# Performance work log

Hardware: AMD Instinct MI355X
Metric: run time of the kernel (lower is better)

Reference implementation:

```python
import jax, jax.numpy as jnp
import numpy as np

S, B, H, F, E, K = 2048, 4, 1024, 4096, 8, 2


def setup_inputs() -> dict:
    key = jax.random.key(0)
    k1, k2, k3, k4 = jax.random.split(key, 4)
    scale_h = 1.0 / np.sqrt(H)
    scale_f = 1.0 / np.sqrt(F)
    return {
        "x": jax.random.normal(k1, (S, B, H), dtype=jnp.float32),
        "router_w": jax.random.normal(k2, (H, E), dtype=jnp.float32) * scale_h,
        "w1": jax.random.normal(k3, (E, H, F), dtype=jnp.float32) * scale_h,
        "w2": jax.random.normal(k4, (E, F, H), dtype=jnp.float32) * scale_f,
    }


def reference(x, router_w, w1, w2):
    # x: [S, B, H] (Megatron layout). Flatten to tokens.
    s, b, h = x.shape
    xt = x.reshape(-1, h)                       # [T, H], T = S*B
    # --- TopK router: softmax over expert logits, then top-k probs ---
    logits = xt @ router_w                      # [T, E]
    probs = jax.nn.softmax(logits, axis=-1)     # [T, E]
    top_p, top_i = jax.lax.top_k(probs, K)      # [T, K] each
    # --- Grouped-GEMM expert MLPs + weighted combine ---
    # Loop over the small fixed expert set; each expert applies fc1->gelu->fc2
    # to every token, masked/weighted by its routing probability (math is
    # identical to dispatch/permute/grouped-GEMM/combine in Megatron).
    out = jnp.zeros_like(xt)
    for e in range(E):
        gate_e = jnp.sum(jnp.where(top_i == e, top_p, 0.0), axis=-1)  # [T]
        hidden = jax.nn.gelu(xt @ w1[e], approximate=True)            # [T, F]
        out = out + gate_e[:, None] * (hidden @ w2[e])                # [T, H]
    return out.reshape(s, b, h)
```

## Files before the change

### kernel.cpp

```cpp
#include <hip/hip_runtime.h>
#include <cstdint>
#include <cstddef>

#define T_TOKENS 8192
#define H_DIM    1024
#define F_DIM    4096
#define E_NUM    8

typedef __bf16 bf16x8 __attribute__((ext_vector_type(8)));
typedef float  f32x4  __attribute__((ext_vector_type(4)));
typedef unsigned short ushort8 __attribute__((ext_vector_type(8)));

#define AS_GLOBAL(p) ((const __attribute__((address_space(1))) void*)(p))
#define AS_LDS(p)    ((__attribute__((address_space(3))) void*)(p))

__device__ inline unsigned short f2b(float f) {
  unsigned int u = __float_as_uint(f);
  unsigned int r = (u + 0x7fffu + ((u >> 16) & 1u)) >> 16;
  return (unsigned short)r;
}
__device__ inline float b2f(unsigned short u) {
  return __uint_as_float(((unsigned int)u) << 16);
}
__device__ inline float gelu_fast(float v) {
  float u2 = 1.5957691216057308f * v * (1.0f + 0.044715f * v * v);
  return v / (1.0f + __expf(-u2));
}

__global__ __launch_bounds__(256) void transpose_cast_kernel(
    const float* __restrict__ in, unsigned short* __restrict__ out, int R, int C)
{
  __shared__ float tile[64][65];
  const int e  = blockIdx.z;
  const int c0 = blockIdx.x * 64;
  const int r0 = blockIdx.y * 64;
  const float* src = in + (size_t)e * R * C;
  unsigned short* dst = out + (size_t)e * R * C;
  const int tid = threadIdx.x;
  const int rl  = tid >> 4;
  const int cl4 = (tid & 15) * 4;
#pragma unroll
  for (int i = 0; i < 4; ++i) {
    float4 v = *(const float4*)(src + (size_t)(r0 + rl + i * 16) * C + c0 + cl4);
    tile[rl + i * 16][cl4 + 0] = v.x;
    tile[rl + i * 16][cl4 + 1] = v.y;
    tile[rl + i * 16][cl4 + 2] = v.z;
    tile[rl + i * 16][cl4 + 3] = v.w;
  }
  __syncthreads();
  const int cl = tid >> 2;
  const int rb = (tid & 3) * 16;
#pragma unroll
  for (int j = 0; j < 4; ++j) {
    ushort4 u;
    u.x = f2b(tile[rb + j * 4 + 0][cl]);
    u.y = f2b(tile[rb + j * 4 + 1][cl]);
    u.z = f2b(tile[rb + j * 4 + 2][cl]);
    u.w = f2b(tile[rb + j * 4 + 3][cl]);
    *(ushort4*)(dst + (size_t)(c0 + cl) * R + r0 + rb + j * 4) = u;
  }
}

__global__ void zero_meta_kernel(int* __restrict__ counts) {
  if (threadIdx.x < 24) counts[threadIdx.x] = 0;
}

__global__ __launch_bounds__(256) void router_kernel(
    const float* __restrict__ x, const float* __restrict__ rw,
    unsigned short* __restrict__ xb, int* __restrict__ top_e, float* __restrict__ top_p,
    int* __restrict__ counts)
{
  __shared__ float lrw[H_DIM * 9];
  __shared__ int lc[E_NUM];
  const int tid = threadIdx.x;
  if (tid < E_NUM) lc[tid] = 0;
  for (int r = tid; r < H_DIM; r += 256) {
    const float* s = rw + r * 8;
    float4 a = *(const float4*)(s);
    float4 b = *(const float4*)(s + 4);
    float* d = &lrw[r * 9];
    d[0] = a.x; d[1] = a.y; d[2] = a.z; d[3] = a.w;
    d[4] = b.x; d[5] = b.y; d[6] = b.z; d[7] = b.w;
  }
  __syncthreads();
  const int lane = tid & 63, wid = tid >> 6;
  for (int i = 0; i < 8; ++i) {
    const int t = blockIdx.x * 32 + wid * 8 + i;
    float acc[8] = {0.f, 0.f, 0.f, 0.f, 0.f, 0.f, 0.f, 0.f};
    const float* xrow = x + (size_t)t * H_DIM;
    unsigned short* xbrow = xb + (size_t)t * H_DIM;
#pragma unroll
    for (int j = 0; j < 16; ++j) {
      int h = j * 64 + lane;
      float xv = xrow[h];
      xbrow[h] = f2b(xv);
      const float* rr = &lrw[h * 9];
#pragma unroll
      for (int e = 0; e < 8; ++e) acc[e] += xv * rr[e];
    }
#pragma unroll
    for (int e = 0; e < 8; ++e) {
#pragma unroll
      for (int s = 32; s > 0; s >>= 1) acc[e] += __shfl_xor(acc[e], s, 64);
    }
    if (lane == 0) {
      float mx = acc[0];
      for (int e = 1; e < 8; ++e) mx = fmaxf(mx, acc[e]);
      float p[8]; float sum = 0.f;
      for (int e = 0; e < 8; ++e) { p[e] = expf(acc[e] - mx); sum += p[e]; }
      float inv = 1.0f / sum;
      int i1 = 0; float b1 = p[0];
      for (int e = 1; e < 8; ++e) if (p[e] > b1) { b1 = p[e]; i1 = e; }
      int i2 = (i1 == 0) ? 1 : 0; float b2 = p[i2];
      for (int e = 0; e < 8; ++e) if (e != i1 && p[e] > b2) { b2 = p[e]; i2 = e; }
      top_e[2 * t]     = i1; top_p[2 * t]     = b1 * inv;
      top_e[2 * t + 1] = i2; top_p[2 * t + 1] = b2 * inv;
      atomicAdd(&lc[i1], 1);
      atomicAdd(&lc[i2], 1);
    }
  }
  __syncthreads();
  if (tid < E_NUM) atomicAdd(&counts[tid], lc[tid]);
}

__global__ void offsets_kernel(const int* __restrict__ counts,
                               int* __restrict__ offsets, int* __restrict__ cursor) {
  if (threadIdx.x == 0) {
    int o = 0;
    for (int e = 0; e < E_NUM; ++e) { offsets[e] = o; o += counts[e]; cursor[e] = 0; }
  }
}

__global__ __launch_bounds__(256) void assign_kernel(
    const int* __restrict__ top_e, const float* __restrict__ top_p,
    const int* __restrict__ offsets, int* __restrict__ cursor,
    int* __restrict__ map, float* __restrict__ gate, int* __restrict__ slot_of)
{
  __shared__ int lc[E_NUM], lb[E_NUM];
  const int tid = threadIdx.x;
  const int t = blockIdx.x * 256 + tid;
  if (tid < E_NUM) lc[tid] = 0;
  __syncthreads();
  int e0 = top_e[2 * t], e1 = top_e[2 * t + 1];
  int p0 = atomicAdd(&lc[e0], 1);
  int p1 = atomicAdd(&lc[e1], 1);
  __syncthreads();
  if (tid < E_NUM) lb[tid] = atomicAdd(&cursor[tid], lc[tid]);
  __syncthreads();
  int s0 = offsets[e0] + lb[e0] + p0;
  int s1 = offsets[e1] + lb[e1] + p1;
  map[s0] = t; gate[s0] = top_p[2 * t];
  map[s1] = t; gate[s1] = top_p[2 * t + 1];
  slot_of[2 * t] = s0; slot_of[2 * t + 1] = s1;
}

template <int KD, int ND, bool USE_MAP, bool GELU>
__global__ __launch_bounds__(256) void moe_gemm_kernel(
    const unsigned short* __restrict__ A, const unsigned short* __restrict__ Bt,
    const int* __restrict__ map, const float* __restrict__ gate,
    const int* __restrict__ counts, const int* __restrict__ offsets,
    unsigned short* __restrict__ C)
{
  __shared__ unsigned short ls[32768];
  const int e   = blockIdx.x;
  const int cnt = counts[e];
  const int tile_m = blockIdx.y;
  if (tile_m * 128 >= cnt) return;
  const int off    = offsets[e];
  const int tile_n = blockIdx.z;
  const int tid    = threadIdx.x;

  const unsigned short* aSrc[4];
  const unsigned short* bSrc[4];
  const int cswz = ((tid & 7) ^ ((tid >> 3) & 7)) * 8;
#pragma unroll
  for (int it = 0; it < 4; ++it) {
    int r  = it * 32 + (tid >> 3);
    int rm = tile_m * 128 + r;
    if (rm > cnt - 1) rm = cnt - 1;
    int arow = USE_MAP ? map[off + rm] : (off + rm);
    aSrc[it] = A + (size_t)arow * KD + cswz;
    int rn = tile_n * 128 + r;
    bSrc[it] = Bt + (size_t)e * ND * KD + (size_t)rn * KD + cswz;
  }

  const int lane = tid & 63;
  const int wid  = tid >> 6;
  const int wm = wid >> 1, wn = wid & 1;
  const int lr = lane & 15, kg = lane >> 4;
  const int swz = lr & 7;

  f32x4 acc[4][4];
#pragma unroll
  for (int mi = 0; mi < 4; ++mi)
#pragma unroll
    for (int ni = 0; ni < 4; ++ni) acc[mi][ni] = (f32x4){0.f, 0.f, 0.f, 0.f};

  constexpr int NK = KD / 64;

#pragma unroll
  for (int it = 0; it < 4; ++it)
    __builtin_amdgcn_global_load_lds(AS_GLOBAL(aSrc[it]),
                                     AS_LDS(ls + (it * 256 + tid) * 8), 16, 0, 0);
#pragma unroll
  for (int it = 0; it < 4; ++it)
    __builtin_amdgcn_global_load_lds(AS_GLOBAL(bSrc[it]),
                                     AS_LDS(ls + 16384 + (it * 256 + tid) * 8), 16, 0, 0);

#pragma unroll 1
  for (int k = 0; k < NK; ++k) {
    const int p = k & 1;
    asm volatile("s_barrier" ::: "memory");
    if (k + 1 < NK) {
      const int q = p ^ 1;
      const int k0 = (k + 1) * 64;
#pragma unroll
      for (int it = 0; it < 4; ++it)
        __builtin_amdgcn_global_load_lds(AS_GLOBAL(aSrc[it] + k0),
                                         AS_LDS(ls + q * 8192 + (it * 256 + tid) * 8), 16, 0, 0);
#pragma unroll
      for (int it = 0; it < 4; ++it)
        __builtin_amdgcn_global_load_lds(AS_GLOBAL(bSrc[it] + k0),
                                         AS_LDS(ls + 16384 + q * 8192 + (it * 256 + tid) * 8), 16, 0, 0);
      asm volatile("s_waitcnt vmcnt(8)" ::: "memory");
    } else {
      asm volatile("s_waitcnt vmcnt(0)" ::: "memory");
    }
    asm volatile("s_barrier" ::: "memory");

    const unsigned short* pA = ls + p * 8192 + (wm * 64 + lr) * 64;
    const unsigned short* pB = ls + 16384 + p * 8192 + (wn * 64 + lr) * 64;
#pragma unroll
    for (int ks = 0; ks < 2; ++ks) {
      bf16x8 aF[4], bF[4];
#pragma unroll
      for (int i = 0; i < 4; ++i)
        aF[i] = *(const bf16x8*)(pA + i * 16 * 64 + (((ks * 4 + kg) ^ swz) * 8));
#pragma unroll
      for (int i = 0; i < 4; ++i)
        bF[i] = *(const bf16x8*)(pB + i * 16 * 64 + (((ks * 4 + kg) ^ swz) * 8));
#pragma unroll
      for (int mi = 0; mi < 4; ++mi)
#pragma unroll
        for (int ni = 0; ni < 4; ++ni)
          acc[mi][ni] = __builtin_amdgcn_mfma_f32_16x16x32_bf16(aF[mi], bF[ni],
                                                                acc[mi][ni], 0, 0, 0);
    }
  }

  __syncthreads();
#pragma unroll
  for (int mi = 0; mi < 4; ++mi) {
#pragma unroll
    for (int r = 0; r < 4; ++r) {
      int Rl = wm * 64 + mi * 16 + kg * 4 + r;
      float gv = 1.0f;
      if (!GELU) {
        int gm = tile_m * 128 + Rl;
        int gmc = gm < cnt ? gm : cnt - 1;
        gv = gate[off + gmc];
      }
#pragma unroll
      for (int ni = 0; ni < 4; ++ni) {
        int col = wn * 64 + ni * 16 + lr;
        float v = acc[mi][ni][r];
        v = GELU ? gelu_fast(v) : v * gv;
        ls[Rl * 136 + col] = f2b(v);
      }
    }
  }
  __syncthreads();
#pragma unroll
  for (int it = 0; it < 8; ++it) {
    int g = it * 256 + tid;
    int R = g >> 4, c16 = g & 15;
    int gm = tile_m * 128 + R;
    if (gm < cnt) {
      ushort8 v = *(const ushort8*)(ls + R * 136 + c16 * 8);
      *(ushort8*)(C + (size_t)(off + gm) * ND + tile_n * 128 + c16 * 8) = v;
    }
  }
}

__global__ __launch_bounds__(256) void combine_kernel(
    const unsigned short* __restrict__ y, const int* __restrict__ slot_of,
    float* __restrict__ out)
{
  const int t  = blockIdx.x;
  const int h0 = threadIdx.x * 4;
  const int s0 = slot_of[2 * t], s1 = slot_of[2 * t + 1];
  ushort4 a = *(const ushort4*)(y + (size_t)s0 * H_DIM + h0);
  ushort4 b = *(const ushort4*)(y + (size_t)s1 * H_DIM + h0);
  float4 o;
  o.x = b2f(a.x) + b2f(b.x);
  o.y = b2f(a.y) + b2f(b.y);
  o.z = b2f(a.z) + b2f(b.z);
  o.w = b2f(a.w) + b2f(b.w);
  *(float4*)(out + (size_t)t * H_DIM + h0) = o;
}

extern "C" void kernel_launch(void* const* d_in, const int* in_sizes, int n_in,
                              void* d_out, int out_size, void* d_ws, size_t ws_size,
                              hipStream_t stream) {
  const float* x  = (const float*)d_in[0];
  const float* rw = (const float*)d_in[1];
  const float* w1 = (const float*)d_in[2];
  const float* w2 = (const float*)d_in[3];
  float* out = (float*)d_out;

  char* ws = (char*)d_ws;
  unsigned short* wT     = (unsigned short*)ws;
  unsigned short* xb     = (unsigned short*)(ws + (64ull  << 20));
  unsigned short* y      = (unsigned short*)(ws + (64ull  << 20));
  unsigned short* hidden = (unsigned short*)(ws + (96ull  << 20));
  char* meta = ws + (224ull << 20);
  int*   top_e   = (int*)meta;
  float* top_p   = (float*)(meta + (64 << 10));
  int*   map     = (int*)(meta + (128 << 10));
  float* gate    = (float*)(meta + (192 << 10));
  int*   slot_of = (int*)(meta + (256 << 10));
  int*   counts  = (int*)(meta + (320 << 10));
  int*   offsets = counts + 8;
  int*   cursor  = counts + 16;

  zero_meta_kernel<<<1, 64, 0, stream>>>(counts);
  transpose_cast_kernel<<<dim3(F_DIM / 64, H_DIM / 64, E_NUM), 256, 0, stream>>>(w1, wT, H_DIM, F_DIM);
  router_kernel<<<256, 256, 0, stream>>>(x, rw, xb, top_e, top_p, counts);
  offsets_kernel<<<1, 64, 0, stream>>>(counts, offsets, cursor);
  assign_kernel<<<T_TOKENS / 256, 256, 0, stream>>>(top_e, top_p, offsets, cursor, map, gate, slot_of);
  moe_gemm_kernel<H_DIM, F_DIM, true, true>
      <<<dim3(E_NUM, 64, F_DIM / 128), 256, 0, stream>>>(xb, wT, map, nullptr, counts, offsets, hidden);
  transpose_cast_kernel<<<dim3(H_DIM / 64, F_DIM / 64, E_NUM), 256, 0, stream>>>(w2, wT, F_DIM, H_DIM);
  moe_gemm_kernel<F_DIM, H_DIM, false, false>
      <<<dim3(E_NUM, 64, H_DIM / 128), 256, 0, stream>>>(hidden, wT, nullptr, gate, counts, offsets, y);
  combine_kernel<<<T_TOKENS, 256, 0, stream>>>(y, slot_of, out);
}
```

Baseline: 751.2 us.

## Enlarge expert GEMM tiles to 256x256 with 512 threads and two-phase epilogue

The grouped expert GEMM moves from 128x128 tiles on 4 waves to 256x256 tiles on 8 waves. Each wave now computes 128x64, with a 2x unrolled double-buffered K loop and an epilogue that stages the output through LDS in two row halves. This raises data reuse per loaded byte, at the cost of 128KB LDS per block, more accumulator registers and fewer blocks. Separately, the weight transpose now writes 16-byte vectors and the router is spread over 4x more blocks. The M grid drops to 20 tiles per expert, which caps coverage at 5120 tokens per expert and would drop rows if routing were more skewed.

```diff
diff --git a/kernel.cpp b/kernel.cpp
--- a/kernel.cpp
+++ b/kernel.cpp
@@ -48,16 +48,15 @@
     tile[rl + i * 16][cl4 + 3] = v.w;
   }
   __syncthreads();
-  const int cl = tid >> 2;
-  const int rb = (tid & 3) * 16;
-#pragma unroll
-  for (int j = 0; j < 4; ++j) {
-    ushort4 u;
-    u.x = f2b(tile[rb + j * 4 + 0][cl]);
-    u.y = f2b(tile[rb + j * 4 + 1][cl]);
-    u.z = f2b(tile[rb + j * 4 + 2][cl]);
-    u.w = f2b(tile[rb + j * 4 + 3][cl]);
-    *(ushort4*)(dst + (size_t)(c0 + cl) * R + r0 + rb + j * 4) = u;
+#pragma unroll
+  for (int it = 0; it < 2; ++it) {
+    int g   = it * 256 + tid;
+    int cl  = g >> 3;
+    int rch = g & 7;
+    ushort8 u;
+#pragma unroll
+    for (int j = 0; j < 8; ++j) u[j] = f2b(tile[rch * 8 + j][cl]);
+    *(ushort8*)(dst + (size_t)(c0 + cl) * R + r0 + rch * 8) = u;
   }
 }
 
@@ -84,8 +83,8 @@
   }
   __syncthreads();
   const int lane = tid & 63, wid = tid >> 6;
-  for (int i = 0; i < 8; ++i) {
-    const int t = blockIdx.x * 32 + wid * 8 + i;
+  for (int i = 0; i < 2; ++i) {
+    const int t = blockIdx.x * 8 + wid * 2 + i;
     float acc[8] = {0.f, 0.f, 0.f, 0.f, 0.f, 0.f, 0.f, 0.f};
     const float* xrow = x + (size_t)t * H_DIM;
     unsigned short* xbrow = xb + (size_t)t * H_DIM;
@@ -155,17 +154,17 @@
 }
 
 template <int KD, int ND, bool USE_MAP, bool GELU>
-__global__ __launch_bounds__(256) void moe_gemm_kernel(
+__global__ __launch_bounds__(512, 2) void moe_gemm_kernel(
     const unsigned short* __restrict__ A, const unsigned short* __restrict__ Bt,
     const int* __restrict__ map, const float* __restrict__ gate,
     const int* __restrict__ counts, const int* __restrict__ offsets,
     unsigned short* __restrict__ C)
 {
-  __shared__ unsigned short ls[32768];
+  __shared__ unsigned short ls[65536];
   const int e   = blockIdx.x;
   const int cnt = counts[e];
   const int tile_m = blockIdx.y;
-  if (tile_m * 128 >= cnt) return;
+  if (tile_m * 256 >= cnt) return;
   const int off    = offsets[e];
   const int tile_n = blockIdx.z;
   const int tid    = threadIdx.x;
@@ -175,110 +174,124 @@
   const int cswz = ((tid & 7) ^ ((tid >> 3) & 7)) * 8;
 #pragma unroll
   for (int it = 0; it < 4; ++it) {
-    int r  = it * 32 + (tid >> 3);
-    int rm = tile_m * 128 + r;
+    int r  = it * 64 + (tid >> 3);
+    int rm = tile_m * 256 + r;
     if (rm > cnt - 1) rm = cnt - 1;
     int arow = USE_MAP ? map[off + rm] : (off + rm);
     aSrc[it] = A + (size_t)arow * KD + cswz;
-    int rn = tile_n * 128 + r;
+    int rn = tile_n * 256 + r;
     bSrc[it] = Bt + (size_t)e * ND * KD + (size_t)rn * KD + cswz;
   }
 
   const int lane = tid & 63;
   const int wid  = tid >> 6;
-  const int wm = wid >> 1, wn = wid & 1;
+  const int wm = wid >> 2, wn = wid & 3;
   const int lr = lane & 15, kg = lane >> 4;
   const int swz = lr & 7;
 
-  f32x4 acc[4][4];
-#pragma unroll
-  for (int mi = 0; mi < 4; ++mi)
+  f32x4 acc[8][4];
+#pragma unroll
+  for (int mi = 0; mi < 8; ++mi)
 #pragma unroll
     for (int ni = 0; ni < 4; ++ni) acc[mi][ni] = (f32x4){0.f, 0.f, 0.f, 0.f};
 
   constexpr int NK = KD / 64;
 
-#pragma unroll
-  for (int it = 0; it < 4; ++it)
-    __builtin_amdgcn_global_load_lds(AS_GLOBAL(aSrc[it]),
-                                     AS_LDS(ls + (it * 256 + tid) * 8), 16, 0, 0);
-#pragma unroll
-  for (int it = 0; it < 4; ++it)
-    __builtin_amdgcn_global_load_lds(AS_GLOBAL(bSrc[it]),
-                                     AS_LDS(ls + 16384 + (it * 256 + tid) * 8), 16, 0, 0);
-
+#define ISSUE_LOADS(kq, buf)                                                   \
+  {                                                                            \
+    const int k0_ = (kq) * 64;                                                 \
+    _Pragma("unroll")                                                          \
+    for (int it = 0; it < 4; ++it)                                             \
+      __builtin_amdgcn_global_load_lds(AS_GLOBAL(aSrc[it] + k0_),              \
+          AS_LDS(ls + (buf) * 16384 + (it * 512 + tid) * 8), 16, 0, 0);        \
+    _Pragma("unroll")                                                          \
+    for (int it = 0; it < 4; ++it)                                             \
+      __builtin_amdgcn_global_load_lds(AS_GLOBAL(bSrc[it] + k0_),              \
+          AS_LDS(ls + 32768 + (buf) * 16384 + (it * 512 + tid) * 8), 16, 0, 0);\
+  }
+
+#define COMPUTE(buf)                                                           \
+  {                                                                            \
+    const unsigned short* pA = ls + (buf) * 16384 + (wm * 128 + lr) * 64;      \
+    const unsigned short* pB = ls + 32768 + (buf) * 16384 + (wn * 64 + lr) * 64;\
+    _Pragma("unroll")                                                          \
+    for (int ks = 0; ks < 2; ++ks) {                                           \
+      const int co = ((ks * 4 + kg) ^ swz) * 8;                                \
+      bf16x8 aF[8], bF[4];                                                     \
+      _Pragma("unroll")                                                        \
+      for (int i = 0; i < 8; ++i) aF[i] = *(const bf16x8*)(pA + i * 16 * 64 + co);\
+      _Pragma("unroll")                                                        \
+      for (int i = 0; i < 4; ++i) bF[i] = *(const bf16x8*)(pB + i * 16 * 64 + co);\
+      _Pragma("unroll")                                                        \
+      for (int mi = 0; mi < 8; ++mi)                                           \
+        _Pragma("unroll")                                                      \
+        for (int ni = 0; ni < 4; ++ni)                                         \
+          acc[mi][ni] = __builtin_amdgcn_mfma_f32_16x16x32_bf16(               \
+              aF[mi], bF[ni], acc[mi][ni], 0, 0, 0);                           \
+    }                                                                          \
+  }
+
+  ISSUE_LOADS(0, 0);
 #pragma unroll 1
-  for (int k = 0; k < NK; ++k) {
-    const int p = k & 1;
+  for (int k = 0; k < NK; k += 2) {
     asm volatile("s_barrier" ::: "memory");
     if (k + 1 < NK) {
-      const int q = p ^ 1;
-      const int k0 = (k + 1) * 64;
-#pragma unroll
-      for (int it = 0; it < 4; ++it)
-        __builtin_amdgcn_global_load_lds(AS_GLOBAL(aSrc[it] + k0),
-                                         AS_LDS(ls + q * 8192 + (it * 256 + tid) * 8), 16, 0, 0);
-#pragma unroll
-      for (int it = 0; it < 4; ++it)
-        __builtin_amdgcn_global_load_lds(AS_GLOBAL(bSrc[it] + k0),
-                                         AS_LDS(ls + 16384 + q * 8192 + (it * 256 + tid) * 8), 16, 0, 0);
+      ISSUE_LOADS(k + 1, 1);
       asm volatile("s_waitcnt vmcnt(8)" ::: "memory");
     } else {
       asm volatile("s_waitcnt vmcnt(0)" ::: "memory");
     }
     asm volatile("s_barrier" ::: "memory");
-
-    const unsigned short* pA = ls + p * 8192 + (wm * 64 + lr) * 64;
-    const unsigned short* pB = ls + 16384 + p * 8192 + (wn * 64 + lr) * 64;
-#pragma unroll
-    for (int ks = 0; ks < 2; ++ks) {
-      bf16x8 aF[4], bF[4];
-#pragma unroll
-      for (int i = 0; i < 4; ++i)
-        aF[i] = *(const bf16x8*)(pA + i * 16 * 64 + (((ks * 4 + kg) ^ swz) * 8));
-#pragma unroll
-      for (int i = 0; i < 4; ++i)
-        bF[i] = *(const bf16x8*)(pB + i * 16 * 64 + (((ks * 4 + kg) ^ swz) * 8));
-#pragma unroll
-      for (int mi = 0; mi < 4; ++mi)
-#pragma unroll
-        for (int ni = 0; ni < 4; ++ni)
-          acc[mi][ni] = __builtin_amdgcn_mfma_f32_16x16x32_bf16(aF[mi], bF[ni],
-                                                                acc[mi][ni], 0, 0, 0);
-    }
-  }
-
-  __syncthreads();
-#pragma unroll
-  for (int mi = 0; mi < 4; ++mi) {
-#pragma unroll
-    for (int r = 0; r < 4; ++r) {
-      int Rl = wm * 64 + mi * 16 + kg * 4 + r;
-      float gv = 1.0f;
-      if (!GELU) {
-        int gm = tile_m * 128 + Rl;
-        int gmc = gm < cnt ? gm : cnt - 1;
-        gv = gate[off + gmc];
+    COMPUTE(0);
+    asm volatile("s_barrier" ::: "memory");
+    if (k + 2 < NK) {
+      ISSUE_LOADS(k + 2, 0);
+      asm volatile("s_waitcnt vmcnt(8)" ::: "memory");
+    } else {
+      asm volatile("s_waitcnt vmcnt(0)" ::: "memory");
+    }
+    asm volatile("s_barrier" ::: "memory");
+    COMPUTE(1);
+  }
+#undef ISSUE_LOADS
+#undef COMPUTE
+
+  __syncthreads();
+#pragma unroll 1
+  for (int ph = 0; ph < 2; ++ph) {
+    if (wm == ph) {
+#pragma unroll
+      for (int mi = 0; mi < 8; ++mi) {
+#pragma unroll
+        for (int r = 0; r < 4; ++r) {
+          int lrow = mi * 16 + kg * 4 + r;
+          float gv = 1.0f;
+          if (!GELU) {
+            int gm = tile_m * 256 + ph * 128 + lrow;
+            gv = gate[off + (gm < cnt ? gm : cnt - 1)];
+          }
+#pragma unroll
+          for (int ni = 0; ni < 4; ++ni) {
+            int col = wn * 64 + ni * 16 + lr;
+            float v = acc[mi][ni][r];
+            v = GELU ? gelu_fast(v) : v * gv;
+            ls[lrow * 264 + col] = f2b(v);
+          }
+        }
       }
-#pragma unroll
-      for (int ni = 0; ni < 4; ++ni) {
-        int col = wn * 64 + ni * 16 + lr;
-        float v = acc[mi][ni][r];
-        v = GELU ? gelu_fast(v) : v * gv;
-        ls[Rl * 136 + col] = f2b(v);
+    }
+    __syncthreads();
+#pragma unroll
+    for (int ps = 0; ps < 8; ++ps) {
+      int g = ps * 512 + tid;
+      int R = g >> 5, c32 = g & 31;
+      int gm = tile_m * 256 + ph * 128 + R;
+      if (gm < cnt) {
+        ushort8 v = *(const ushort8*)(ls + R * 264 + c32 * 8);
+        *(ushort8*)(C + (size_t)(off + gm) * ND + tile_n * 256 + c32 * 8) = v;
       }
     }
-  }
-  __syncthreads();
-#pragma unroll
-  for (int it = 0; it < 8; ++it) {
-    int g = it * 256 + tid;
-    int R = g >> 4, c16 = g & 15;
-    int gm = tile_m * 128 + R;
-    if (gm < cnt) {
-      ushort8 v = *(const ushort8*)(ls + R * 136 + c16 * 8);
-      *(ushort8*)(C + (size_t)(off + gm) * ND + tile_n * 128 + c16 * 8) = v;
-    }
+    __syncthreads();
   }
 }
 
@@ -325,13 +338,13 @@
 
   zero_meta_kernel<<<1, 64, 0, stream>>>(counts);
   transpose_cast_kernel<<<dim3(F_DIM / 64, H_DIM / 64, E_NUM), 256, 0, stream>>>(w1, wT, H_DIM, F_DIM);
-  router_kernel<<<256, 256, 0, stream>>>(x, rw, xb, top_e, top_p, counts);
+  router_kernel<<<1024, 256, 0, stream>>>(x, rw, xb, top_e, top_p, counts);
   offsets_kernel<<<1, 64, 0, stream>>>(counts, offsets, cursor);
   assign_kernel<<<T_TOKENS / 256, 256, 0, stream>>>(top_e, top_p, offsets, cursor, map, gate, slot_of);
   moe_gemm_kernel<H_DIM, F_DIM, true, true>
-      <<<dim3(E_NUM, 64, F_DIM / 128), 256, 0, stream>>>(xb, wT, map, nullptr, counts, offsets, hidden);
+      <<<dim3(E_NUM, 20, F_DIM / 256), 512, 0, stream>>>(xb, wT, map, nullptr, counts, offsets, hidden);
   transpose_cast_kernel<<<dim3(H_DIM / 64, F_DIM / 64, E_NUM), 256, 0, stream>>>(w2, wT, F_DIM, H_DIM);
   moe_gemm_kernel<F_DIM, H_DIM, false, false>
-      <<<dim3(E_NUM, 64, H_DIM / 128), 256, 0, stream>>>(hidden, wT, nullptr, gate, counts, offsets, y);
+      <<<dim3(E_NUM, 20, H_DIM / 256), 512, 0, stream>>>(hidden, wT, nullptr, gate, counts, offsets, y);
   combine_kernel<<<T_TOKENS, 256, 0, stream>>>(y, slot_of, out);
 }
```

After: 807.1 us. 1.07x slower.
